# Kernel optimization log

Measured on AMD Instinct MI355X. Metric: run time of the kernel, lower is better.

Reference implementation:

```python
import jax, jax.numpy as jnp
import numpy as np

B, S, H = 2, 2048, 2048
NH, NKV, HD = 32, 8, 64
GROUPS = NH // NKV
SCALE = HD ** -0.5


def _rope_tables(key):
    # Real RoPE cos/sin tables (HF Llama style), shape [B, S, HD]
    inv_freq = 1.0 / (10000.0 ** (jnp.arange(0, HD, 2, dtype=jnp.float32) / HD))  # [HD/2]
    t = jnp.arange(S, dtype=jnp.float32)
    freqs = jnp.outer(t, inv_freq)                      # [S, HD/2]
    emb = jnp.concatenate([freqs, freqs], axis=-1)      # [S, HD]
    cos = jnp.broadcast_to(jnp.cos(emb)[None], (B, S, HD))
    sin = jnp.broadcast_to(jnp.sin(emb)[None], (B, S, HD))
    return cos, sin


def setup_inputs() -> dict:
    key = jax.random.key(0)
    ks = jax.random.split(key, 9)
    w = 0.02
    cos, sin = _rope_tables(key)
    return {
        "hidden_states": jax.random.normal(ks[0], (B, S, H), jnp.float32),
        "bounding_box_embeddings": jax.random.normal(ks[1], (B, S, H), jnp.float32),
        "cos": cos,
        "sin": sin,
        "Wq": jax.random.normal(ks[2], (H, NH * HD), jnp.float32) * w,
        "Wk": jax.random.normal(ks[3], (H, NKV * HD), jnp.float32) * w,
        "Wv": jax.random.normal(ks[4], (H, NKV * HD), jnp.float32) * w,
        "Wo": jax.random.normal(ks[5], (NH * HD, H), jnp.float32) * w,
        "Wsq": jax.random.normal(ks[6], (H, NH * HD), jnp.float32) * w,
        "Wsk": jax.random.normal(ks[7], (H, NKV * HD), jnp.float32) * w,
    }


def _rotate_half(x):
    x1, x2 = x[..., : HD // 2], x[..., HD // 2 :]
    return jnp.concatenate([-x2, x1], axis=-1)


def _apply_rope(q, k, cos, sin):
    # q: [B,NH,S,HD], k: [B,NKV,S,HD]; cos/sin [B,S,HD] -> broadcast over heads
    c = cos[:, None, :, :]
    s = sin[:, None, :, :]
    return q * c + _rotate_half(q) * s, k * c + _rotate_half(k) * s


def _proj_heads(x, W, n_heads):
    b, s, _ = x.shape
    return (x @ W).reshape(b, s, n_heads, HD).transpose(0, 2, 1, 3)  # [B,nh,S,HD]


def reference(hidden_states, bounding_box_embeddings, cos, sin, Wq, Wk, Wv, Wo, Wsq, Wsk):
    # Text Q/K/V with RoPE
    q = _proj_heads(hidden_states, Wq, NH)
    k = _proj_heads(hidden_states, Wk, NKV)
    v = _proj_heads(hidden_states, Wv, NKV)
    q, k = _apply_rope(q, k, cos, sin)
    # Spatial Q/K (no V) with RoPE
    sq = _proj_heads(bounding_box_embeddings, Wsq, NH)
    sk = _proj_heads(bounding_box_embeddings, Wsk, NKV)
    sq, sk = _apply_rope(sq, sk, cos, sin)
    # Fused text+spatial states, then GQA repeat_kv
    q = q + sq                                   # [B,NH,S,HD]
    k = jnp.repeat(k + sk, GROUPS, axis=1)       # [B,NH,S,HD]
    v = jnp.repeat(v, GROUPS, axis=1)            # [B,NH,S,HD]
    # Eager attention with causal mask
    scores = jnp.einsum("bhqd,bhkd->bhqk", q, k) * SCALE
    causal = jnp.tril(jnp.ones((S, S), dtype=bool))
    scores = jnp.where(causal[None, None], scores, jnp.finfo(jnp.float32).min)
    probs = jax.nn.softmax(scores.astype(jnp.float32), axis=-1).astype(q.dtype)
    attn = jnp.einsum("bhqk,bhkd->bhqd", probs, v)           # [B,NH,S,HD]
    attn = attn.transpose(0, 2, 1, 3).reshape(B, S, NH * HD)  # [B,S,NH*HD]
    return attn @ Wo
```

## Files before the change

kernel.cpp:

```cpp
#include <hip/hip_runtime.h>

#define B_ 2
#define S_ 2048
#define H_ 2048
#define NH_ 32
#define NKV_ 8
#define HD_ 64

typedef short short8 __attribute__((ext_vector_type(8)));
typedef float f32x4 __attribute__((ext_vector_type(4)));
typedef float f32x16 __attribute__((ext_vector_type(16)));
typedef unsigned int uint4v __attribute__((ext_vector_type(4)));

__device__ __forceinline__ float bf2f(unsigned short u) {
  union { unsigned int i; float f; } v; v.i = ((unsigned int)u) << 16; return v.f;
}
__device__ __forceinline__ unsigned short f2bf(float f) {
  union { float f; unsigned int i; } v; v.f = f;
  unsigned int u = v.i;
  u += 0x7fffu + ((u >> 16) & 1u);
  return (unsigned short)(u >> 16);
}
__device__ __forceinline__ unsigned int cvtpk(float lo, float hi) {
  unsigned int r;
  asm("v_cvt_pk_bf16_f32 %0, %1, %2" : "=v"(r) : "v"(lo), "v"(hi));
  return r;
}
__device__ __forceinline__ void pl32swap(unsigned int& a, unsigned int& b) {
  asm("v_permlane32_swap_b32 %0, %1" : "+v"(a), "+v"(b));
}
__device__ __forceinline__ short8 mkfrag(unsigned a, unsigned b, unsigned c, unsigned d) {
  union { uint4v u; short8 s; } x;
  x.u = (uint4v){a, b, c, d};
  return x.s;
}
__device__ __forceinline__ void gload_lds16(const unsigned short* g, unsigned short* l) {
  __builtin_amdgcn_global_load_lds((const __attribute__((address_space(1))) void*)g,
                                   (__attribute__((address_space(3))) void*)l,
                                   16, 0, 0);
}
#define MFMA32(A, B, C) __builtin_amdgcn_mfma_f32_32x32x16_bf16(A, B, C, 0, 0, 0)
#define BARF() asm volatile("s_barrier" ::: "memory")

__global__ __launch_bounds__(256) void cast_f32_bf16(const float* __restrict__ in,
                                                     unsigned short* __restrict__ out,
                                                     int n8) {
  int i = blockIdx.x * 256 + threadIdx.x;
  if (i >= n8) return;
  float4 v0 = ((const float4*)in)[i * 2];
  float4 v1 = ((const float4*)in)[i * 2 + 1];
  ushort4 o0, o1;
  o0.x = f2bf(v0.x); o0.y = f2bf(v0.y); o0.z = f2bf(v0.z); o0.w = f2bf(v0.w);
  o1.x = f2bf(v1.x); o1.y = f2bf(v1.y); o1.z = f2bf(v1.z); o1.w = f2bf(v1.w);
  ((ushort4*)out)[i * 2] = o0;
  ((ushort4*)out)[i * 2 + 1] = o1;
}

__global__ __launch_bounds__(256) void transpose_cast(const float* __restrict__ W,
                                                      unsigned short* __restrict__ Wt,
                                                      int N, int K) {
  __shared__ float tile[32][33];
  int n0 = blockIdx.x * 32, k0 = blockIdx.y * 32;
  int tx = threadIdx.x & 31;
  int ty = threadIdx.x >> 5;
#pragma unroll
  for (int i = 0; i < 32; i += 8)
    tile[ty + i][tx] = W[(size_t)(k0 + ty + i) * N + n0 + tx];
  __syncthreads();
#pragma unroll
  for (int i = 0; i < 32; i += 8)
    Wt[(size_t)(n0 + ty + i) * K + k0 + tx] = f2bf(tile[tx][ty + i]);
}

__global__ __launch_bounds__(256) void vtrans_kernel(const unsigned short* __restrict__ P1,
                                                     unsigned short* __restrict__ Vt) {
  __shared__ unsigned short tile[32][33];
  int s0 = blockIdx.x * 32, d0 = blockIdx.y * 32, bk = blockIdx.z;
  int b = bk >> 3, kv = bk & 7;
  int tx = threadIdx.x & 31, ty = threadIdx.x >> 5;
#pragma unroll
  for (int i = 0; i < 32; i += 8)
    tile[ty + i][tx] = P1[(size_t)(b * S_ + s0 + ty + i) * 3072 + 2560 + kv * 64 + d0 + tx];
  __syncthreads();
#pragma unroll
  for (int i = 0; i < 32; i += 8)
    Vt[(size_t)(bk * 64 + d0 + ty + i) * S_ + s0 + tx] = tile[tx][ty + i];
}

__global__ __launch_bounds__(256) void combine_rope(const unsigned short* __restrict__ P1,
                                                    const unsigned short* __restrict__ P2,
                                                    const float* __restrict__ cosT,
                                                    const float* __restrict__ sinT,
                                                    unsigned short* __restrict__ Qb,
                                                    unsigned short* __restrict__ Kb) {
  int id = blockIdx.x * 256 + threadIdx.x;
  int row = id / 640;
  int grp = id - row * 640;
  int b = row >> 11;
  int s = row & 2047;
  bool isQ = grp < 512;
  int n = isQ ? grp * 4 : (grp - 512) * 4;
  int h = n >> 6;
  int d = n & 63;
  int base = isQ ? 0 : 2048;
  const int ld1 = 3072, ld2 = 2560;
  int pd = (d < 32) ? d + 32 : d - 32;
  float sign = (d < 32) ? -1.f : 1.f;
  int pcol = base + h * 64 + pd;

  ushort4 a1 = *(const ushort4*)&P1[(size_t)row * ld1 + base + n];
  ushort4 a2 = *(const ushort4*)&P2[(size_t)row * ld2 + base + n];
  ushort4 b1 = *(const ushort4*)&P1[(size_t)row * ld1 + pcol];
  ushort4 b2 = *(const ushort4*)&P2[(size_t)row * ld2 + pcol];
  float4 cv = *(const float4*)&cosT[(size_t)row * 64 + d];
  float4 sv = *(const float4*)&sinT[(size_t)row * 64 + d];
  float scale = isQ ? 0.125f : 1.0f;

  float xs[4] = { bf2f(a1.x) + bf2f(a2.x), bf2f(a1.y) + bf2f(a2.y),
                  bf2f(a1.z) + bf2f(a2.z), bf2f(a1.w) + bf2f(a2.w) };
  float xp[4] = { bf2f(b1.x) + bf2f(b2.x), bf2f(b1.y) + bf2f(b2.y),
                  bf2f(b1.z) + bf2f(b2.z), bf2f(b1.w) + bf2f(b2.w) };
  float cc[4] = { cv.x, cv.y, cv.z, cv.w };
  float ss[4] = { sv.x, sv.y, sv.z, sv.w };
  ushort4 o;
  unsigned short* op = (unsigned short*)&o;
#pragma unroll
  for (int i = 0; i < 4; ++i)
    op[i] = f2bf((xs[i] * cc[i] + sign * xp[i] * ss[i]) * scale);

  if (isQ)
    *(ushort4*)&Qb[((size_t)(b * NH_ + h) * S_ + s) * HD_ + d] = o;
  else
    *(ushort4*)&Kb[((size_t)(b * NKV_ + h) * S_ + s) * HD_ + d] = o;
}


#define RD_A(BC, MH) do { \
  _Pragma("unroll") for (int mf = 0; mf < 4; ++mf) { \
    _Pragma("unroll") for (int ks = 0; ks < 2; ++ks) \
      a[mf][ks] = *(const short8*)&lds[BC][((wm * 2 + (MH)) * 8 + mf * 2 + ks) * 512 + l * 8]; \
  } \
} while (0)

#define RD_B(BC, NH, DST) do { \
  _Pragma("unroll") for (int nf = 0; nf < 2; ++nf) { \
    _Pragma("unroll") for (int ks = 0; ks < 2; ++ks) \
      DST[nf][ks] = *(const short8*)&lds[BC][16384 + (((wn * 2 + (NH)) * 2 + nf) * 2 + ks) * 512 + l * 8]; \
  } \
} while (0)

#define MM(MH, NH, BB) do { \
  _Pragma("unroll") for (int mf = 0; mf < 4; ++mf) { \
    _Pragma("unroll") for (int nf = 0; nf < 2; ++nf) { \
      _Pragma("unroll") for (int ks = 0; ks < 2; ++ks) \
        acc[(MH) * 4 + mf][(NH) * 2 + nf] = __builtin_amdgcn_mfma_f32_16x16x32_bf16( \
            a[mf][ks], BB[nf][ks], acc[(MH) * 4 + mf][(NH) * 2 + nf], 0, 0, 0); \
    } \
  } \
} while (0)

#define STAGE_A(H, KT) do { \
  int bq_ = (KT) & 1; \
  gload_lds16(srcA0 + (size_t)(H) * (64 * 2048) + (KT) * 64, &lds[bq_][((H) * 8 + w) * 512]); \
  gload_lds16(srcA1 + (size_t)(H) * (64 * 2048) + (KT) * 64, &lds[bq_][(16 + (H) * 8 + w) * 512]); \
} while (0)

#define STAGE_B(H, KT) do { \
  int bq_ = (KT) & 1; \
  gload_lds16(srcB0 + (size_t)(H) * (32 * 2048) + (KT) * 64, \
              &lds[bq_][16384 + ((w >> 2) * 8 + (H) * 4 + (w & 3)) * 512]); \
  gload_lds16(srcB1 + (size_t)(H) * (32 * 2048) + (KT) * 64, \
              &lds[bq_][16384 + (16 + (w >> 2) * 8 + (H) * 4 + (w & 3)) * 512]); \
} while (0)

#define GROUP_P(BC, G) do { \
  int kt1 = (G) + 1; if (kt1 > 31) kt1 = 31; \
  int kt2 = (G) + 2; if (kt2 > 31) kt2 = 31; \
  int BN_ = kt1 & 1; \
   \
  BARF(); \
  __builtin_amdgcn_s_setprio(1); MM(0, 0, b0); __builtin_amdgcn_s_setprio(0); \
  RD_B(BC, 1, b1); \
  STAGE_A(1, kt1); \
   \
  BARF(); \
  __builtin_amdgcn_s_setprio(1); MM(0, 1, b1); __builtin_amdgcn_s_setprio(0); \
  STAGE_A(0, kt2); \
   \
  BARF(); \
  RD_A(BC, 1); \
  __builtin_amdgcn_s_setprio(1); MM(1, 0, b0); __builtin_amdgcn_s_setprio(0); \
  STAGE_B(0, kt2); \
  asm volatile("s_waitcnt vmcnt(8)" ::: "memory"); \
   \
  BARF(); \
  __builtin_amdgcn_s_setprio(1); MM(1, 1, b1); __builtin_amdgcn_s_setprio(0); \
  RD_A(BN_, 0); \
  RD_B(BN_, 0, b0); \
  STAGE_B(1, kt2); \
  asm volatile("s_waitcnt vmcnt(6)" ::: "memory"); \
} while (0)

template <int OF32>
__global__ __launch_bounds__(512, 2) void gemm256(const unsigned short* __restrict__ A,
                                                  const unsigned short* __restrict__ Bt,
                                                  void* __restrict__ Cv,
                                                  int N, int nbx) {
  __shared__ unsigned short lds[2][32768];
  int nwg = gridDim.x;
  int orig = blockIdx.x;
  int wgid = (orig & 7) * (nwg >> 3) + (orig >> 3);
  int bn = wgid % nbx, bm = wgid / nbx;
  int t = threadIdx.x, w = t >> 6, l = t & 63;
  int wm = w >> 2, wn = w & 3;

  int kcol = (w & 1) * 32 + ((t >> 4) & 3) * 8;
  int rA0 = bm * 256 + ((w >> 1) & 3) * 16 + (t & 15);
  const unsigned short* srcA0 = A + (size_t)rA0 * 2048 + kcol;
  const unsigned short* srcA1 = srcA0 + (size_t)128 * 2048;
  int nB0 = bn * 256 + (w >> 2) * 64 + ((w >> 1) & 1) * 16 + (t & 15);
  const unsigned short* srcB0 = Bt + (size_t)nB0 * 2048 + kcol;
  const unsigned short* srcB1 = srcB0 + (size_t)128 * 2048;

  short8 a[4][2], b0[2][2], b1[2][2];
  f32x4 acc[8][4];
#pragma unroll
  for (int mi = 0; mi < 8; ++mi)
#pragma unroll
    for (int ni = 0; ni < 4; ++ni) acc[mi][ni] = 0.f;

  STAGE_A(0, 0); STAGE_A(1, 0); STAGE_B(0, 0); STAGE_B(1, 0);
  STAGE_A(0, 1); STAGE_B(0, 1); STAGE_B(1, 1);
  asm volatile("s_waitcnt vmcnt(6)" ::: "memory");
  BARF();
  RD_A(0, 0);
  RD_B(0, 0, b0);

  for (int tg = 0; tg < 32; tg += 2) {
    GROUP_P(0, tg);
    GROUP_P(1, tg + 1);
  }
  asm volatile("s_waitcnt vmcnt(0)" ::: "memory");

#pragma unroll
  for (int mi = 0; mi < 8; ++mi) {
    int row = bm * 256 + wm * 128 + (mi >> 2) * 64 + (mi & 3) * 16 + (l >> 4) * 4;
#pragma unroll
    for (int ni = 0; ni < 4; ++ni) {
      int col = bn * 256 + wn * 64 + (ni >> 1) * 32 + (ni & 1) * 16 + (l & 15);
#pragma unroll
      for (int r = 0; r < 4; ++r) {
        if constexpr (OF32)
          ((float*)Cv)[(size_t)(row + r) * N + col] = acc[mi][ni][r];
        else
          ((unsigned short*)Cv)[(size_t)(row + r) * N + col] = f2bf(acc[mi][ni][r]);
      }
    }
  }
}

#define RD_BN(BC) do { \
  _Pragma("unroll") for (int nf = 0; nf < 2; ++nf) { \
    _Pragma("unroll") for (int ks = 0; ks < 2; ++ks) \
      bb[nf][ks] = *(const short8*)&lds2[BC][16384 + ((wn * 2 + nf) * 2 + ks) * 512 + l * 8]; \
  } \
} while (0)

#define RD_AN(BC, MH) do { \
  _Pragma("unroll") for (int mf = 0; mf < 4; ++mf) { \
    _Pragma("unroll") for (int ks = 0; ks < 2; ++ks) \
      a[mf][ks] = *(const short8*)&lds2[BC][((wm * 2 + (MH)) * 8 + mf * 2 + ks) * 512 + l * 8]; \
  } \
} while (0)

#define MMN(MH) do { \
  _Pragma("unroll") for (int mf = 0; mf < 4; ++mf) { \
    _Pragma("unroll") for (int nf = 0; nf < 2; ++nf) { \
      _Pragma("unroll") for (int ks = 0; ks < 2; ++ks) \
        acc[(MH) * 4 + mf][nf] = __builtin_amdgcn_mfma_f32_16x16x32_bf16( \
            a[mf][ks], bb[nf][ks], acc[(MH) * 4 + mf][nf], 0, 0, 0); \
    } \
  } \
} while (0)

#define STAGE_AU(Q, KT) do { \
  int bq_ = (KT) & 1; \
  gload_lds16((((Q) < 2) ? srcA0 : srcA1) + (size_t)((Q) & 1) * (64 * 2048) + (size_t)(KT) * 64, \
              &lds2[bq_][(((Q) >> 1) * 16 + ((Q) & 1) * 8 + w) * 512]); \
} while (0)

#define STAGE_BU(H, KT) do { \
  int bq_ = (KT) & 1; \
  gload_lds16(srcB0 + (size_t)(H) * (32 * 2048) + (size_t)(KT) * 64, \
              &lds2[bq_][16384 + ((w >> 2) * 8 + (H) * 4 + (w & 3)) * 512]); \
} while (0)

#define GROUPN(BC, G) do { \
  int kt1 = (G) + 1; if (kt1 > 31) kt1 = 31; \
  int kt2 = (G) + 2; if (kt2 > 31) kt2 = 31; \
  RD_AN(BC, 0); RD_BN(BC); \
  STAGE_AU(1, kt1); STAGE_AU(3, kt1); \
  BARF(); \
  __builtin_amdgcn_s_setprio(1); MMN(0); __builtin_amdgcn_s_setprio(0); \
  BARF(); \
  RD_AN(BC, 1); \
  STAGE_AU(0, kt2); STAGE_AU(2, kt2); STAGE_BU(0, kt2); STAGE_BU(1, kt2); \
  BARF(); \
  __builtin_amdgcn_s_setprio(1); MMN(1); __builtin_amdgcn_s_setprio(0); \
  asm volatile("s_waitcnt vmcnt(4)" ::: "memory"); \
  BARF(); \
} while (0)

__global__ __launch_bounds__(512, 2) void gemm256n(const unsigned short* __restrict__ A,
                                                   const unsigned short* __restrict__ Bt,
                                                   float* __restrict__ C,
                                                   int N, int nbx) {
  __shared__ unsigned short lds2[2][24576];
  int nwg = gridDim.x;
  int orig = blockIdx.x;
  int wgid = (orig & 7) * (nwg >> 3) + (orig >> 3);
  int bn = wgid % nbx, bm = wgid / nbx;
  int t = threadIdx.x, w = t >> 6, l = t & 63;
  int wm = w >> 2, wn = w & 3;

  int kcol = (w & 1) * 32 + ((t >> 4) & 3) * 8;
  int rA0 = bm * 256 + ((w >> 1) & 3) * 16 + (t & 15);
  const unsigned short* srcA0 = A + (size_t)rA0 * 2048 + kcol;
  const unsigned short* srcA1 = srcA0 + (size_t)128 * 2048;
  int nB0 = bn * 128 + (w >> 2) * 64 + ((w >> 1) & 1) * 16 + (t & 15);
  const unsigned short* srcB0 = Bt + (size_t)nB0 * 2048 + kcol;

  short8 a[4][2], bb[2][2];
  f32x4 acc[8][2];
#pragma unroll
  for (int mi = 0; mi < 8; ++mi)
#pragma unroll
    for (int ni = 0; ni < 2; ++ni) acc[mi][ni] = 0.f;

  STAGE_AU(0, 0); STAGE_AU(1, 0); STAGE_AU(2, 0); STAGE_AU(3, 0); STAGE_BU(0, 0); STAGE_BU(1, 0);
  STAGE_AU(0, 1); STAGE_AU(2, 1); STAGE_BU(0, 1); STAGE_BU(1, 1);
  asm volatile("s_waitcnt vmcnt(4)" ::: "memory");
  BARF();

  for (int tg = 0; tg < 32; tg += 2) {
    GROUPN(0, tg);
    GROUPN(1, tg + 1);
  }
  asm volatile("s_waitcnt vmcnt(0)" ::: "memory");

#pragma unroll
  for (int mi = 0; mi < 8; ++mi) {
    int row = bm * 256 + wm * 128 + (mi >> 2) * 64 + (mi & 3) * 16 + (l >> 4) * 4;
#pragma unroll
    for (int nf = 0; nf < 2; ++nf) {
      int col = bn * 128 + wn * 32 + nf * 16 + (l & 15);
#pragma unroll
      for (int r = 0; r < 4; ++r)
        C[(size_t)(row + r) * N + col] = acc[mi][nf][r];
    }
  }
}

__global__ __launch_bounds__(512) void attn_kernel(const unsigned short* __restrict__ Q,
                                                   const unsigned short* __restrict__ K,
                                                   const unsigned short* __restrict__ Vt,
                                                   unsigned short* __restrict__ attnOut) {
  __shared__ unsigned short lK[2][64 * 64];
  __shared__ unsigned short lV[2][64 * 64];

  int bx = blockIdx.x;
  int j = bx & 7;
  int bh = bx >> 3;
  int head = bh & 31;
  int b = bh >> 5;
  int kvh = head >> 2;
  const unsigned short* Kp = K + (size_t)(b * NKV_ + kvh) * S_ * HD_;
  const unsigned short* Vp = Vt + (size_t)(b * NKV_ + kvh) * HD_ * S_;

  int t = threadIdx.x;
  int w = t >> 6, l = t & 63;
  int q32 = l & 31, hf = l >> 5;
  int qb_eff = (w < 4) ? j : (15 - j);
  int qbase_w = qb_eff * 128 + (w & 3) * 32;
  const unsigned short* Qp = Q + ((size_t)(b * NH_ + head) * S_ + qbase_w) * HD_;

  short8 qf[4];
  {
    const unsigned short* qrow = Qp + (size_t)q32 * HD_ + hf * 8;
#pragma unroll
    for (int kc = 0; kc < 4; ++kc)
      qf[kc] = *(const short8*)(qrow + kc * 16);
  }

  int srow = t >> 3;
  int sslot = t & 7;
  unsigned lOff = srow * 128 + ((sslot ^ (srow & 7)) << 4);
  const char* gK0 = (const char*)(Kp + (size_t)srow * 64 + sslot * 8);
  const char* gV0 = (const char*)(Vp + (size_t)srow * 2048 + sslot * 8);

  {
    int4 rk = *(const int4*)(gK0);
    int4 rv = *(const int4*)(gV0);
    *(int4*)((char*)lK[0] + lOff) = rk;
    *(int4*)((char*)lV[0] + lOff) = rv;
  }
  __syncthreads();

  f32x16 oA = 0.f, oB = 0.f;
  float mrun = -1e30f, lrun = 0.f;

  int nt = 32 - 2 * j;
  int cur = 0;
  for (int tI = 0; tI < nt; ++tI) {
    int kv0 = tI * 64;
    bool pf = (tI + 1 < nt);
    int4 nk, nv;
    if (pf) {
      nk = *(const int4*)(gK0 + (size_t)(kv0 + 64) * 128);
      nv = *(const int4*)(gV0 + (size_t)(kv0 + 64) * 2);
    }

    if (kv0 <= qbase_w + 31) {
      const char* lKc = (const char*)lK[cur];
      const char* lVc = (const char*)lV[cur];
      int swz = q32 & 7;

      f32x16 sA = 0.f, sB = 0.f;
      __builtin_amdgcn_s_setprio(1);
#pragma unroll
      for (int kc = 0; kc < 4; ++kc) {
        int cs = (kc << 1) | hf;
        short8 ak0 = *(const short8*)(lKc + q32 * 128 + ((cs ^ swz) << 4));
        short8 ak1 = *(const short8*)(lKc + (32 + q32) * 128 + ((cs ^ swz) << 4));
        sA = MFMA32(ak0, qf[kc], sA);
        sB = MFMA32(ak1, qf[kc], sB);
      }
      __builtin_amdgcn_s_setprio(0);

      if (kv0 + 63 > qbase_w) {
        int qg = qbase_w + q32;
#pragma unroll
        for (int r = 0; r < 16; ++r) {
          int kvr = kv0 + (r & 3) + ((r >> 2) << 3) + (hf << 2);
          if (kvr > qg) sA[r] = -1e30f;
          if (kvr + 32 > qg) sB[r] = -1e30f;
        }
      }

      float pmax = sA[0];
#pragma unroll
      for (int r = 1; r < 16; ++r) pmax = fmaxf(pmax, sA[r]);
#pragma unroll
      for (int r = 0; r < 16; ++r) pmax = fmaxf(pmax, sB[r]);
      pmax = fmaxf(pmax, __shfl_xor(pmax, 32, 64));

      if (!__all(pmax <= mrun + 8.f)) {
        float mnew = fmaxf(mrun, pmax);
        float sf = __expf(mrun - mnew);
        lrun *= sf;
        mrun = mnew;
#pragma unroll
        for (int r = 0; r < 16; ++r) {
          int src = (r & 3) + ((r >> 2) << 3) + (hf << 2);
          float sfr = __shfl(sf, src, 64);
          oA[r] *= sfr;
          oB[r] *= sfr;
        }
      }

      float rs = 0.f;
#pragma unroll
      for (int r = 0; r < 16; ++r) { sA[r] = __expf(sA[r] - mrun); rs += sA[r]; }
#pragma unroll
      for (int r = 0; r < 16; ++r) { sB[r] = __expf(sB[r] - mrun); rs += sB[r]; }
      rs += __shfl_xor(rs, 32, 64);
      lrun += rs;

      short8 paf[4];
      {
        unsigned c0 = cvtpk(sA[0], sA[1]), c1 = cvtpk(sA[2], sA[3]);
        unsigned c2 = cvtpk(sA[4], sA[5]), c3 = cvtpk(sA[6], sA[7]);
        pl32swap(c0, c2); pl32swap(c1, c3);
        paf[0] = mkfrag(c0, c1, c2, c3);
      }
      {
        unsigned c0 = cvtpk(sA[8], sA[9]),  c1 = cvtpk(sA[10], sA[11]);
        unsigned c2 = cvtpk(sA[12], sA[13]), c3 = cvtpk(sA[14], sA[15]);
        pl32swap(c0, c2); pl32swap(c1, c3);
        paf[1] = mkfrag(c0, c1, c2, c3);
      }
      {
        unsigned c0 = cvtpk(sB[0], sB[1]), c1 = cvtpk(sB[2], sB[3]);
        unsigned c2 = cvtpk(sB[4], sB[5]), c3 = cvtpk(sB[6], sB[7]);
        pl32swap(c0, c2); pl32swap(c1, c3);
        paf[2] = mkfrag(c0, c1, c2, c3);
      }
      {
        unsigned c0 = cvtpk(sB[8], sB[9]),  c1 = cvtpk(sB[10], sB[11]);
        unsigned c2 = cvtpk(sB[12], sB[13]), c3 = cvtpk(sB[14], sB[15]);
        pl32swap(c0, c2); pl32swap(c1, c3);
        paf[3] = mkfrag(c0, c1, c2, c3);
      }

      __builtin_amdgcn_s_setprio(1);
#pragma unroll
      for (int ks = 0; ks < 4; ++ks) {
        int cs = (ks << 1) | hf;
        short8 v0 = *(const short8*)(lVc + q32 * 128 + ((cs ^ swz) << 4));
        short8 v1 = *(const short8*)(lVc + (32 + q32) * 128 + ((cs ^ swz) << 4));
        oA = MFMA32(paf[ks], v0, oA);
        oB = MFMA32(paf[ks], v1, oB);
      }
      __builtin_amdgcn_s_setprio(0);
    }

    if (pf) {
      *(int4*)((char*)lK[cur ^ 1] + lOff) = nk;
      *(int4*)((char*)lV[cur ^ 1] + lOff) = nv;
    }
    __syncthreads();
    cur ^= 1;
  }

  float linv = 1.f / lrun;
#pragma unroll
  for (int r = 0; r < 16; ++r) {
    int src = (r & 3) + ((r >> 2) << 3) + (hf << 2);
    float li = __shfl(linv, src, 64);
    unsigned short* op = attnOut + ((size_t)(b * S_ + qbase_w + src)) * (NH_ * HD_) + head * 64;
    op[q32] = f2bf(oA[r] * li);
    op[32 + q32] = f2bf(oB[r] * li);
  }
}

extern "C" void kernel_launch(void* const* d_in, const int* in_sizes, int n_in,
                              void* d_out, int out_size, void* d_ws, size_t ws_size,
                              hipStream_t stream) {
  const float* hidden = (const float*)d_in[0];
  const float* bbox   = (const float*)d_in[1];
  const float* cosT   = (const float*)d_in[2];
  const float* sinT   = (const float*)d_in[3];
  const float* Wq  = (const float*)d_in[4];
  const float* Wk  = (const float*)d_in[5];
  const float* Wv  = (const float*)d_in[6];
  const float* Wo  = (const float*)d_in[7];
  const float* Wsq = (const float*)d_in[8];
  const float* Wsk = (const float*)d_in[9];

  char* ws = (char*)d_ws;
  size_t off = 0;
  auto alloc = [&](size_t bytes) {
    void* p = ws + off;
    off += (bytes + 255) & ~(size_t)255;
    return p;
  };
  unsigned short* WhT = (unsigned short*)alloc((size_t)3072 * 2048 * 2);
  unsigned short* WbT = (unsigned short*)alloc((size_t)2560 * 2048 * 2);
  unsigned short* WoT = (unsigned short*)alloc((size_t)2048 * 2048 * 2);
  unsigned short* P1  = (unsigned short*)alloc((size_t)4096 * 3072 * 2);
  unsigned short* P2  = (unsigned short*)alloc((size_t)4096 * 2560 * 2);
  unsigned short* Xh  = (unsigned short*)alloc((size_t)4096 * 2048 * 2);
  unsigned short* Xb  = (unsigned short*)alloc((size_t)4096 * 2048 * 2);
  unsigned short* attn = Xh;
  unsigned short* Qb   = Xb;
  unsigned short* Kb   = Xb + (size_t)B_ * NH_ * S_ * HD_;
  unsigned short* Vt   = Kb + (size_t)B_ * NKV_ * S_ * HD_;

  dim3 blk(256);
  cast_f32_bf16<<<dim3(4096), blk, 0, stream>>>(hidden, Xh, 4096 * 2048 / 8);
  cast_f32_bf16<<<dim3(4096), blk, 0, stream>>>(bbox,   Xb, 4096 * 2048 / 8);

  transpose_cast<<<dim3(64, 64), blk, 0, stream>>>(Wq,  WhT, 2048, 2048);
  transpose_cast<<<dim3(16, 64), blk, 0, stream>>>(Wk,  WhT + (size_t)2048 * 2048, 512, 2048);
  transpose_cast<<<dim3(16, 64), blk, 0, stream>>>(Wv,  WhT + (size_t)2560 * 2048, 512, 2048);
  transpose_cast<<<dim3(64, 64), blk, 0, stream>>>(Wsq, WbT, 2048, 2048);
  transpose_cast<<<dim3(16, 64), blk, 0, stream>>>(Wsk, WbT + (size_t)2048 * 2048, 512, 2048);
  transpose_cast<<<dim3(64, 64), blk, 0, stream>>>(Wo,  WoT, 2048, 2048);

  gemm256<0><<<dim3(192), dim3(512), 0, stream>>>(Xh, WhT, P1, 3072, 12);
  gemm256<0><<<dim3(160), dim3(512), 0, stream>>>(Xb, WbT, P2, 2560, 10);

  combine_rope<<<dim3((B_ * S_ * 640) / 256), blk, 0, stream>>>(P1, P2, cosT, sinT, Qb, Kb);
  vtrans_kernel<<<dim3(64, 2, 16), blk, 0, stream>>>(P1, Vt);

  attn_kernel<<<dim3(512), dim3(512), 0, stream>>>(Qb, Kb, Vt, attn);

  gemm256n<<<dim3(256), dim3(512), 0, stream>>>(attn, WoT, (float*)d_out, 2048, 16);
}
```

Before: 303.5 us.

## Pre-pack GEMM operands into fragment-tiled layout during fp32-to-bf16 cast

The cast kernels now write activations and the QKV/spatial weights directly in the 512-element fragment order the projection GEMM stages into LDS. Each global-to-LDS load becomes one contiguous 1 KB chunk instead of strided rows. The three weight transposes per projection are merged into a single castW_frag launch. The cost is reshuffled reads in the cast kernels and changed workspace aliasing, which must not clobber buffers still in use.

```diff
diff --git a/kernel.cpp b/kernel.cpp
--- a/kernel.cpp
+++ b/kernel.cpp
@@ -42,18 +42,56 @@
 #define MFMA32(A, B, C) __builtin_amdgcn_mfma_f32_32x32x16_bf16(A, B, C, 0, 0, 0)
 #define BARF() asm volatile("s_barrier" ::: "memory")
 
-__global__ __launch_bounds__(256) void cast_f32_bf16(const float* __restrict__ in,
-                                                     unsigned short* __restrict__ out,
-                                                     int n8) {
-  int i = blockIdx.x * 256 + threadIdx.x;
-  if (i >= n8) return;
-  float4 v0 = ((const float4*)in)[i * 2];
-  float4 v1 = ((const float4*)in)[i * 2 + 1];
+__global__ __launch_bounds__(256) void castA_frag(const float* __restrict__ in,
+                                                  unsigned short* __restrict__ out) {
+  int c = blockIdx.x * 4 + (threadIdx.x >> 6);
+  int l = threadIdx.x & 63;
+  int D = c & 31, KT = (c >> 5) & 31, bm = c >> 10;
+  int row = bm * 256 + ((D >> 4) & 1) * 128 + ((D >> 3) & 1) * 64 + ((D >> 1) & 3) * 16 + (l & 15);
+  int k = KT * 64 + (D & 1) * 32 + (l >> 4) * 8;
+  const float* src = in + (size_t)row * 2048 + k;
+  float4 v0 = *(const float4*)src;
+  float4 v1 = *(const float4*)(src + 4);
   ushort4 o0, o1;
   o0.x = f2bf(v0.x); o0.y = f2bf(v0.y); o0.z = f2bf(v0.z); o0.w = f2bf(v0.w);
   o1.x = f2bf(v1.x); o1.y = f2bf(v1.y); o1.z = f2bf(v1.z); o1.w = f2bf(v1.w);
-  ((ushort4*)out)[i * 2] = o0;
-  ((ushort4*)out)[i * 2 + 1] = o1;
+  unsigned short* dst = out + (size_t)c * 512 + l * 8;
+  *(ushort4*)dst = o0;
+  *(ushort4*)(dst + 4) = o1;
+}
+
+__global__ __launch_bounds__(256) void castW_frag(const float* __restrict__ W0,
+                                                  const float* __restrict__ W1,
+                                                  const float* __restrict__ W2,
+                                                  unsigned short* __restrict__ out) {
+  __shared__ float tile[64][33];
+  int c = blockIdx.x;
+  int ngroup = c & 7, KT = (c >> 3) & 31, bn = c >> 8;
+  int n0 = bn * 256 + ngroup * 32;
+  const float* W; int Nw, nb;
+  if (n0 < 2048)      { W = W0; Nw = 2048; nb = n0; }
+  else if (n0 < 2560) { W = W1; Nw = 512;  nb = n0 - 2048; }
+  else                { W = W2; Nw = 512;  nb = n0 - 2560; }
+  int t = threadIdx.x;
+  int col = t & 31, r8 = t >> 5;
+#pragma unroll
+  for (int p = 0; p < 8; ++p) {
+    int kk = p * 8 + r8;
+    tile[kk][col] = W[(size_t)(KT * 64 + kk) * Nw + nb + col];
+  }
+  __syncthreads();
+  int e = t >> 6, l = t & 63;
+  int nf = e >> 1, ks = e & 1;
+  ushort4 o0, o1;
+  unsigned short* op = (unsigned short*)&o0;
+#pragma unroll
+  for (int j = 0; j < 8; ++j) {
+    unsigned short v = f2bf(tile[ks * 32 + (l >> 4) * 8 + j][nf * 16 + (l & 15)]);
+    if (j < 4) op[j] = v; else ((unsigned short*)&o1)[j - 4] = v;
+  }
+  unsigned short* dst = out + (((size_t)(c >> 3) * 32 + ngroup * 4 + e) << 9) + l * 8;
+  *(ushort4*)dst = o0;
+  *(ushort4*)(dst + 4) = o1;
 }
 
 __global__ __launch_bounds__(256) void transpose_cast(const float* __restrict__ W,
@@ -161,16 +199,16 @@
 
 #define STAGE_A(H, KT) do { \
   int bq_ = (KT) & 1; \
-  gload_lds16(srcA0 + (size_t)(H) * (64 * 2048) + (KT) * 64, &lds[bq_][((H) * 8 + w) * 512]); \
-  gload_lds16(srcA1 + (size_t)(H) * (64 * 2048) + (KT) * 64, &lds[bq_][(16 + (H) * 8 + w) * 512]); \
+  int d1_ = (H) * 8 + w; \
+  gload_lds16(aF + (((size_t)((KT) * 32 + d1_)) << 9), &lds[bq_][d1_ * 512]); \
+  gload_lds16(aF + (((size_t)((KT) * 32 + 16 + d1_)) << 9), &lds[bq_][(16 + d1_) * 512]); \
 } while (0)
 
 #define STAGE_B(H, KT) do { \
   int bq_ = (KT) & 1; \
-  gload_lds16(srcB0 + (size_t)(H) * (32 * 2048) + (KT) * 64, \
-              &lds[bq_][16384 + ((w >> 2) * 8 + (H) * 4 + (w & 3)) * 512]); \
-  gload_lds16(srcB1 + (size_t)(H) * (32 * 2048) + (KT) * 64, \
-              &lds[bq_][16384 + (16 + (w >> 2) * 8 + (H) * 4 + (w & 3)) * 512]); \
+  int e1_ = (w >> 2) * 8 + (H) * 4 + (w & 3); \
+  gload_lds16(bF + (((size_t)((KT) * 32 + e1_)) << 9), &lds[bq_][16384 + e1_ * 512]); \
+  gload_lds16(bF + (((size_t)((KT) * 32 + 16 + e1_)) << 9), &lds[bq_][16384 + (16 + e1_) * 512]); \
 } while (0)
 
 #define GROUP_P(BC, G) do { \
@@ -202,8 +240,8 @@
 } while (0)
 
 template <int OF32>
-__global__ __launch_bounds__(512, 2) void gemm256(const unsigned short* __restrict__ A,
-                                                  const unsigned short* __restrict__ Bt,
+__global__ __launch_bounds__(512, 2) void gemm256(const unsigned short* __restrict__ Afr,
+                                                  const unsigned short* __restrict__ Wfr,
                                                   void* __restrict__ Cv,
                                                   int N, int nbx) {
   __shared__ unsigned short lds[2][32768];
@@ -214,13 +252,8 @@
   int t = threadIdx.x, w = t >> 6, l = t & 63;
   int wm = w >> 2, wn = w & 3;
 
-  int kcol = (w & 1) * 32 + ((t >> 4) & 3) * 8;
-  int rA0 = bm * 256 + ((w >> 1) & 3) * 16 + (t & 15);
-  const unsigned short* srcA0 = A + (size_t)rA0 * 2048 + kcol;
-  const unsigned short* srcA1 = srcA0 + (size_t)128 * 2048;
-  int nB0 = bn * 256 + (w >> 2) * 64 + ((w >> 1) & 1) * 16 + (t & 15);
-  const unsigned short* srcB0 = Bt + (size_t)nB0 * 2048 + kcol;
-  const unsigned short* srcB1 = srcB0 + (size_t)128 * 2048;
+  const unsigned short* aF = Afr + ((size_t)bm << 19) + l * 8;
+  const unsigned short* bF = Wfr + ((size_t)bn << 19) + l * 8;
 
   short8 a[4][2], b0[2][2], b1[2][2];
   f32x4 acc[8][4];
@@ -554,31 +587,27 @@
     off += (bytes + 255) & ~(size_t)255;
     return p;
   };
-  unsigned short* WhT = (unsigned short*)alloc((size_t)3072 * 2048 * 2);
-  unsigned short* WbT = (unsigned short*)alloc((size_t)2560 * 2048 * 2);
-  unsigned short* WoT = (unsigned short*)alloc((size_t)2048 * 2048 * 2);
-  unsigned short* P1  = (unsigned short*)alloc((size_t)4096 * 3072 * 2);
-  unsigned short* P2  = (unsigned short*)alloc((size_t)4096 * 2560 * 2);
-  unsigned short* Xh  = (unsigned short*)alloc((size_t)4096 * 2048 * 2);
-  unsigned short* Xb  = (unsigned short*)alloc((size_t)4096 * 2048 * 2);
-  unsigned short* attn = Xh;
-  unsigned short* Qb   = Xb;
-  unsigned short* Kb   = Xb + (size_t)B_ * NH_ * S_ * HD_;
-  unsigned short* Vt   = Kb + (size_t)B_ * NKV_ * S_ * HD_;
+  unsigned short* AfrH = (unsigned short*)alloc((size_t)4096 * 2048 * 2);
+  unsigned short* AfrB = (unsigned short*)alloc((size_t)4096 * 2048 * 2);
+  unsigned short* WhF  = (unsigned short*)alloc((size_t)3072 * 2048 * 2);
+  unsigned short* WbF  = (unsigned short*)alloc((size_t)2560 * 2048 * 2);
+  unsigned short* WoT  = (unsigned short*)alloc((size_t)2048 * 2048 * 2);
+  unsigned short* P1   = (unsigned short*)alloc((size_t)4096 * 3072 * 2);
+  unsigned short* P2   = (unsigned short*)alloc((size_t)4096 * 2560 * 2);
+  unsigned short* Qb   = AfrB;
+  unsigned short* Kb   = AfrH;
+  unsigned short* Vt   = AfrH + (size_t)B_ * NKV_ * S_ * HD_;
+  unsigned short* attn = WhF;
 
   dim3 blk(256);
-  cast_f32_bf16<<<dim3(4096), blk, 0, stream>>>(hidden, Xh, 4096 * 2048 / 8);
-  cast_f32_bf16<<<dim3(4096), blk, 0, stream>>>(bbox,   Xb, 4096 * 2048 / 8);
-
-  transpose_cast<<<dim3(64, 64), blk, 0, stream>>>(Wq,  WhT, 2048, 2048);
-  transpose_cast<<<dim3(16, 64), blk, 0, stream>>>(Wk,  WhT + (size_t)2048 * 2048, 512, 2048);
-  transpose_cast<<<dim3(16, 64), blk, 0, stream>>>(Wv,  WhT + (size_t)2560 * 2048, 512, 2048);
-  transpose_cast<<<dim3(64, 64), blk, 0, stream>>>(Wsq, WbT, 2048, 2048);
-  transpose_cast<<<dim3(16, 64), blk, 0, stream>>>(Wsk, WbT + (size_t)2048 * 2048, 512, 2048);
-  transpose_cast<<<dim3(64, 64), blk, 0, stream>>>(Wo,  WoT, 2048, 2048);
-
-  gemm256<0><<<dim3(192), dim3(512), 0, stream>>>(Xh, WhT, P1, 3072, 12);
-  gemm256<0><<<dim3(160), dim3(512), 0, stream>>>(Xb, WbT, P2, 2560, 10);
+  castA_frag<<<dim3(4096), blk, 0, stream>>>(hidden, AfrH);
+  castA_frag<<<dim3(4096), blk, 0, stream>>>(bbox,   AfrB);
+  castW_frag<<<dim3(3072), blk, 0, stream>>>(Wq,  Wk,  Wv,      WhF);
+  castW_frag<<<dim3(2560), blk, 0, stream>>>(Wsq, Wsk, nullptr, WbF);
+  transpose_cast<<<dim3(64, 64), blk, 0, stream>>>(Wo, WoT, 2048, 2048);
+
+  gemm256<0><<<dim3(192), dim3(512), 0, stream>>>(AfrH, WhF, P1, 3072, 12);
+  gemm256<0><<<dim3(160), dim3(512), 0, stream>>>(AfrB, WbF, P2, 2560, 10);
 
   combine_rope<<<dim3((B_ * S_ * 640) / 256), blk, 0, stream>>>(P1, P2, cosT, sinT, Qb, Kb);
   vtrans_kernel<<<dim3(64, 2, 16), blk, 0, stream>>>(P1, Vt);
```

New measurement: 261.9 us. -13.7%, faster.
